# Optimization experiments

Hardware: AMD Instinct MI355X
Metric: run time of the kernel (lower is better)

The kernel has to match this reference:

```python
import jax, jax.numpy as jnp
import numpy as np

N = 100000      # num nodes
E = 1600000     # num edges
DIN, DH, DOUT = 128, 64, 32
BN_EPS = 1e-5


def setup_inputs() -> dict:
    key = jax.random.key(0)
    ks = jax.random.split(key, 6)

    def xavier(k, fi, fo):
        lim = np.sqrt(6.0 / (fi + fo)).astype(np.float32)
        return jax.random.uniform(k, (fi, fo), jnp.float32, -lim, lim)

    return {
        "x": jax.random.normal(ks[0], (N, DIN), jnp.float32),
        "edge_index": jax.random.randint(ks[1], (2, E), 0, N, dtype=jnp.int32),
        "W1": xavier(ks[2], DIN, DH),
        "b1": jnp.zeros((DH,), jnp.float32),
        "gamma1": jnp.ones((DH,), jnp.float32),
        "beta1": jnp.zeros((DH,), jnp.float32),
        "W2": xavier(ks[3], DH, DOUT),
        "b2": jnp.zeros((DOUT,), jnp.float32),
    }


def _gcn_norm(edge_index, n, dtype):
    # add self-loops, then symmetric normalization deg^-1/2[src] * deg^-1/2[dst]
    loop = jnp.arange(n, dtype=edge_index.dtype)
    src = jnp.concatenate([edge_index[0], loop])
    dst = jnp.concatenate([edge_index[1], loop])
    deg = jax.ops.segment_sum(jnp.ones_like(dst, dtype=dtype), dst, num_segments=n)
    dis = 1.0 / jnp.sqrt(deg)  # deg >= 1 due to self-loops
    norm = dis[src] * dis[dst]
    return src, dst, norm


def _gcn_layer(h, W, b, src, dst, norm, n):
    h = h @ W
    msg = h[src] * norm[:, None]                       # [E+N, d] gather
    out = jax.ops.segment_sum(msg, dst, num_segments=n)  # scatter-add
    return out + b


def reference(x, edge_index, W1, b1, gamma1, beta1, W2, b2):
    src, dst, norm = _gcn_norm(edge_index, N, x.dtype)
    # layer 1: GCNConv -> BatchNorm (batch stats) -> ReLU (dropout = eval/identity)
    h = _gcn_layer(x, W1, b1, src, dst, norm, N)
    mean = h.mean(axis=0)
    var = h.var(axis=0)
    h = (h - mean) / jnp.sqrt(var + BN_EPS) * gamma1 + beta1
    h = jax.nn.relu(h)
    # layer 2: GCNConv -> node embeddings [N, DOUT]
    out = _gcn_layer(h, W2, b2, src, dst, norm, N)
    return out
```

## Files before the change

kernel.cpp:

```cpp
#include <hip/hip_runtime.h>

#define DIN 128
#define DH 64
#define DOUT 32
#define BN_EPS 1e-5f

#define BK 128
#define BKSH 7
#define NBK_MAX 784
#define G 512

typedef __attribute__((ext_vector_type(8))) short short8;
typedef __attribute__((ext_vector_type(4))) float floatx4;

__device__ __forceinline__ unsigned short f2bf(float f) {
    union { float f; unsigned u; } v; v.f = f;
    unsigned r = (v.u + 0x7FFFu + ((v.u >> 16) & 1u)) >> 16;
    return (unsigned short)r;
}
__device__ __forceinline__ float bf2f(unsigned short h) {
    union { unsigned u; float f; } v; v.u = ((unsigned)h) << 16;
    return v.f;
}


__global__ __launch_bounds__(256) void wprep_k(const float* __restrict__ W1, const float* __restrict__ W2,
                                               unsigned short* __restrict__ w1t, unsigned short* __restrict__ w2t) {
    int i = blockIdx.x * 256 + threadIdx.x;
    if (i < 8192) {
        int k = i >> 6, nn = i & 63;
        w1t[nn * 128 + k] = f2bf(W1[i]);
    } else if (i < 8192 + 2048) {
        int j = i - 8192;
        int k = j >> 5, nn = j & 31;
        w2t[nn * 64 + k] = f2bf(W2[j]);
    }
}


__global__ __launch_bounds__(256) void hist_k(const int* __restrict__ dst, int* __restrict__ hist_g,
                                              int E, int nbk, int chunk) {
    __shared__ int hist[NBK_MAX];
    int g = blockIdx.x, tid = threadIdx.x;
    for (int b = tid; b < nbk; b += 256) hist[b] = 0;
    __syncthreads();
    int i0 = g * chunk, iend = min(i0 + chunk, E);
    for (int i = i0 + tid; i < iend; i += 256)
        atomicAdd(&hist[dst[i] >> BKSH], 1);
    __syncthreads();
    for (int b = tid; b < nbk; b += 256)
        hist_g[(size_t)g * nbk + b] = hist[b];
}


__global__ __launch_bounds__(256) void scan_k(const int* __restrict__ hist_g, int* __restrict__ rowoff,
                                              int* __restrict__ tot, int nbk) {
    __shared__ int sa[G], sb[G];
    int b = blockIdx.x, tid = threadIdx.x;
    int v0 = hist_g[(size_t)tid * nbk + b];
    int v1 = hist_g[(size_t)(tid + 256) * nbk + b];
    sa[tid] = v0; sa[tid + 256] = v1;
    __syncthreads();
    int* pin = sa; int* pout = sb;
    for (int off = 1; off < G; off <<= 1) {
        int a0 = pin[tid] + ((tid >= off) ? pin[tid - off] : 0);
        int a1 = pin[tid + 256] + ((tid + 256 >= off) ? pin[tid + 256 - off] : 0);
        pout[tid] = a0; pout[tid + 256] = a1;
        __syncthreads();
        int* t = pin; pin = pout; pout = t;
    }
    rowoff[(size_t)b * G + tid] = pin[tid] - v0;
    rowoff[(size_t)b * G + tid + 256] = pin[tid + 256] - v1;
    if (tid == 0) tot[b] = pin[G - 1];
}


__global__ __launch_bounds__(1024) void base_k(const int* __restrict__ tot, int* __restrict__ base,
                                               int nbk, int E) {
    __shared__ int sa[1024], sb[1024];
    int tid = threadIdx.x;
    int v = (tid < nbk) ? tot[tid] : 0;
    sa[tid] = v;
    __syncthreads();
    int* pin = sa; int* pout = sb;
    for (int off = 1; off < 1024; off <<= 1) {
        int a = pin[tid] + ((tid >= off) ? pin[tid - off] : 0);
        pout[tid] = a;
        __syncthreads();
        int* t = pin; pin = pout; pout = t;
    }
    if (tid < nbk) base[tid] = pin[tid] - v;
    if (tid == 0) base[nbk] = E;
}


__global__ __launch_bounds__(256) void scatter_k(const int* __restrict__ src, const int* __restrict__ dst,
                                                 const int* __restrict__ base, const int* __restrict__ rowoff,
                                                 unsigned* __restrict__ recs, int E, int nbk, int chunk) {
    __shared__ int cur[NBK_MAX];
    int g = blockIdx.x, tid = threadIdx.x;
    for (int b = tid; b < nbk; b += 256)
        cur[b] = base[b] + rowoff[(size_t)b * G + g];
    __syncthreads();
    int i0 = g * chunk, iend = min(i0 + chunk, E);
    for (int i = i0 + tid; i < iend; i += 256) {
        int s = src[i], d = dst[i];
        int b = d >> BKSH;
        int slot = atomicAdd(&cur[b], 1);
        recs[slot] = ((unsigned)s << BKSH) | (unsigned)(d & (BK - 1));
    }
}


__global__ __launch_bounds__(256) void csr_k(const unsigned* __restrict__ recs, const int* __restrict__ base,
                                             float* __restrict__ dis, int2* __restrict__ rpde,
                                             int* __restrict__ col, int n) {
    __shared__ int deg[BK], bas[BK], cur[BK], sc[BK];
    int b = blockIdx.x, tid = threadIdx.x;
    if (tid < BK) { deg[tid] = 0; cur[tid] = 0; }
    __syncthreads();
    int lo = base[b], hi = base[b + 1];
    for (int e = lo + tid; e < hi; e += 256)
        atomicAdd(&deg[recs[e] & (BK - 1)], 1);
    __syncthreads();
    if (tid < BK) sc[tid] = deg[tid];
    __syncthreads();
    for (int off = 1; off < BK; off <<= 1) {
        int t = (tid >= off && tid < BK) ? sc[tid - off] : 0;
        __syncthreads();
        if (tid < BK) sc[tid] += t;
        __syncthreads();
    }
    if (tid < BK) {
        bas[tid] = sc[tid] - deg[tid];
        int g = b * BK + tid;
        if (g < n) {
            dis[g] = rsqrtf((float)(deg[tid] + 1));
            rpde[g] = make_int2(lo + bas[tid], deg[tid]);
        }
    }
    __syncthreads();
    for (int e = lo + tid; e < hi; e += 256) {
        unsigned r = recs[e];
        int dl = r & (BK - 1);
        int k = atomicAdd(&cur[dl], 1);
        col[lo + bas[dl] + k] = (int)(r >> BKSH);
    }
}


__global__ __launch_bounds__(256) void gemm1_k(const float* __restrict__ x,
                                               const unsigned short* __restrict__ w1t,
                                               const float* __restrict__ dis,
                                               unsigned short* __restrict__ h1s, int n) {
    __shared__ unsigned short xb[64][136];
    __shared__ unsigned short wt[64][136];
    int tid = threadIdx.x;
    int r0b = blockIdx.x * 64;

    for (int c = tid; c < 1024; c += 256) {
        int nn = c >> 4, kc = (c & 15) * 8;
        *(short8*)&wt[nn][kc] = *(const short8*)&w1t[nn * 128 + kc];
    }
    for (int c = tid; c < 2048; c += 256) {
        int r = c >> 5, k4 = (c & 31) * 4;
        int gr = r0b + r;
        float4 v = make_float4(0.f, 0.f, 0.f, 0.f);
        if (gr < n) v = ((const float4*)x)[(gr << 5) + (k4 >> 2)];
        ushort4 o;
        o.x = f2bf(v.x); o.y = f2bf(v.y); o.z = f2bf(v.z); o.w = f2bf(v.w);
        *(ushort4*)&xb[r][k4] = o;
    }
    __syncthreads();

    int w = tid >> 6, lane = tid & 63;
    int rr = lane & 15, q = lane >> 4;
    floatx4 acc0 = {0.f, 0.f, 0.f, 0.f}, acc1 = acc0, acc2 = acc0, acc3 = acc0;
    #pragma unroll
    for (int kt = 0; kt < 4; kt++) {
        int k0 = kt * 32 + q * 8;
        short8 a  = *(const short8*)&xb[w * 16 + rr][k0];
        short8 b0 = *(const short8*)&wt[rr][k0];
        short8 b1 = *(const short8*)&wt[16 + rr][k0];
        short8 b2 = *(const short8*)&wt[32 + rr][k0];
        short8 b3 = *(const short8*)&wt[48 + rr][k0];
        acc0 = __builtin_amdgcn_mfma_f32_16x16x32_bf16(a, b0, acc0, 0, 0, 0);
        acc1 = __builtin_amdgcn_mfma_f32_16x16x32_bf16(a, b1, acc1, 0, 0, 0);
        acc2 = __builtin_amdgcn_mfma_f32_16x16x32_bf16(a, b2, acc2, 0, 0, 0);
        acc3 = __builtin_amdgcn_mfma_f32_16x16x32_bf16(a, b3, acc3, 0, 0, 0);
    }
    #pragma unroll
    for (int t = 0; t < 4; t++) {
        int gr = r0b + w * 16 + q * 4 + t;
        if (gr < n) {
            float dd = dis[gr];
            unsigned short* o = &h1s[gr * 64];
            o[rr]      = f2bf(acc0[t] * dd);
            o[16 + rr] = f2bf(acc1[t] * dd);
            o[32 + rr] = f2bf(acc2[t] * dd);
            o[48 + rr] = f2bf(acc3[t] * dd);
        }
    }
}


__global__ __launch_bounds__(256) void agg1_k(const unsigned short* __restrict__ h1s,
                                              const int2* __restrict__ rpde,
                                              const int* __restrict__ col,
                                              unsigned short* __restrict__ out, int n) {
    int node = (blockIdx.x * 256 + threadIdx.x) >> 6;
    int f = threadIdx.x & 63;
    if (node >= n) return;
    int2 rd = rpde[node];
    int e  = __builtin_amdgcn_readfirstlane(rd.x);
    int dg = __builtin_amdgcn_readfirstlane(rd.y);
    int ee = e + dg;
    float a0 = 0.f, a1 = 0.f, a2 = 0.f, a3 = 0.f, a4 = 0.f, a5 = 0.f, a6 = 0.f, a7 = 0.f;
    for (; e + 7 < ee; e += 8) {
        int s0 = col[e],     s1 = col[e + 1], s2 = col[e + 2], s3 = col[e + 3];
        int s4 = col[e + 4], s5 = col[e + 5], s6 = col[e + 6], s7 = col[e + 7];
        a0 += bf2f(h1s[s0 * 64 + f]);
        a1 += bf2f(h1s[s1 * 64 + f]);
        a2 += bf2f(h1s[s2 * 64 + f]);
        a3 += bf2f(h1s[s3 * 64 + f]);
        a4 += bf2f(h1s[s4 * 64 + f]);
        a5 += bf2f(h1s[s5 * 64 + f]);
        a6 += bf2f(h1s[s6 * 64 + f]);
        a7 += bf2f(h1s[s7 * 64 + f]);
    }
    for (; e + 3 < ee; e += 4) {
        int s0 = col[e], s1 = col[e + 1], s2 = col[e + 2], s3 = col[e + 3];
        a0 += bf2f(h1s[s0 * 64 + f]);
        a1 += bf2f(h1s[s1 * 64 + f]);
        a2 += bf2f(h1s[s2 * 64 + f]);
        a3 += bf2f(h1s[s3 * 64 + f]);
    }
    for (; e < ee; e++) a0 += bf2f(h1s[col[e] * 64 + f]);
    float dn = rsqrtf((float)(dg + 1));
    float s = ((a0 + a1) + (a2 + a3)) + ((a4 + a5) + (a6 + a7));
    out[node * 64 + f] = f2bf((s + bf2f(h1s[node * 64 + f])) * dn);
}


__global__ __launch_bounds__(256) void bnstats_k(const unsigned short* __restrict__ agg1b,
                                                 float* __restrict__ stats, int n) {
    int f = threadIdx.x & 63, g = threadIdx.x >> 6;
    float sum = 0.f, sq = 0.f;
    for (int r = blockIdx.x * 4 + g; r < n; r += gridDim.x * 4) {
        float v = bf2f(agg1b[r * 64 + f]);
        sum += v; sq += v * v;
    }
    __shared__ float s1[4][64], s2[4][64];
    s1[g][f] = sum; s2[g][f] = sq;
    __syncthreads();
    if (g == 0) {
        sum = s1[0][f] + s1[1][f] + s1[2][f] + s1[3][f];
        sq  = s2[0][f] + s2[1][f] + s2[2][f] + s2[3][f];
        atomicAdd(&stats[f], sum);
        atomicAdd(&stats[64 + f], sq);
    }
}

__global__ __launch_bounds__(64) void bnfin_k(const float* __restrict__ stats, const float* __restrict__ gamma,
                                              const float* __restrict__ beta, float* __restrict__ st, float invn) {
    int f = threadIdx.x;
    if (f < 64) {
        float mean = stats[f] * invn;
        float var = stats[64 + f] * invn - mean * mean;
        float s = gamma[f] * rsqrtf(var + BN_EPS);
        st[f] = s;
        st[64 + f] = beta[f] - mean * s;
    }
}


__global__ __launch_bounds__(256) void gemm2_k(const unsigned short* __restrict__ agg1b,
                                               const unsigned short* __restrict__ w2t,
                                               const float* __restrict__ st, const float* __restrict__ dis,
                                               unsigned short* __restrict__ h2s, int n) {
    __shared__ unsigned short ab[64][72];
    __shared__ unsigned short wt[32][72];
    __shared__ float s_s[64], s_t[64];
    int tid = threadIdx.x;
    int r0b = blockIdx.x * 64;
    if (tid < 64) { s_s[tid] = st[tid]; s_t[tid] = st[64 + tid]; }
    if (tid < 256) {
        int c = tid;
        int nn = c >> 3, kc = (c & 7) * 8;
        *(short8*)&wt[nn][kc] = *(const short8*)&w2t[nn * 64 + kc];
    }
    __syncthreads();
    for (int c = tid; c < 512; c += 256) {
        int r = c >> 3, k0 = (c & 7) * 8;
        int gr = r0b + r;
        unsigned short tmp[8];
        if (gr < n) {
            const unsigned short* ap = &agg1b[gr * 64 + k0];
            #pragma unroll
            for (int j = 0; j < 8; j++)
                tmp[j] = f2bf(fmaxf(bf2f(ap[j]) * s_s[k0 + j] + s_t[k0 + j], 0.f));
        } else {
            #pragma unroll
            for (int j = 0; j < 8; j++) tmp[j] = 0;
        }
        *(short8*)&ab[r][k0] = *(short8*)tmp;
    }
    __syncthreads();

    int w = tid >> 6, lane = tid & 63;
    int rr = lane & 15, q = lane >> 4;
    floatx4 acc0 = {0.f, 0.f, 0.f, 0.f}, acc1 = acc0;
    #pragma unroll
    for (int kt = 0; kt < 2; kt++) {
        int k0 = kt * 32 + q * 8;
        short8 a  = *(const short8*)&ab[w * 16 + rr][k0];
        short8 b0 = *(const short8*)&wt[rr][k0];
        short8 b1 = *(const short8*)&wt[16 + rr][k0];
        acc0 = __builtin_amdgcn_mfma_f32_16x16x32_bf16(a, b0, acc0, 0, 0, 0);
        acc1 = __builtin_amdgcn_mfma_f32_16x16x32_bf16(a, b1, acc1, 0, 0, 0);
    }
    #pragma unroll
    for (int t = 0; t < 4; t++) {
        int gr = r0b + w * 16 + q * 4 + t;
        if (gr < n) {
            float dd = dis[gr];
            h2s[gr * 32 + rr]      = f2bf(acc0[t] * dd);
            h2s[gr * 32 + 16 + rr] = f2bf(acc1[t] * dd);
        }
    }
}


__global__ __launch_bounds__(256) void agg2_k(const unsigned short* __restrict__ h2s,
                                              const int2* __restrict__ rpde,
                                              const int* __restrict__ col, const float* __restrict__ b2,
                                              float* __restrict__ out, int n) {
    int node = (blockIdx.x * 256 + threadIdx.x) >> 6;
    int lane = threadIdx.x & 63;
    if (node >= n) return;
    int f = lane & 31, half = lane >> 5;
    int2 rd = rpde[node];
    int e0 = __builtin_amdgcn_readfirstlane(rd.x);
    int dg = __builtin_amdgcn_readfirstlane(rd.y);
    int e = e0 + half, ee = e0 + dg;
    float a0 = 0.f, a1 = 0.f, a2 = 0.f, a3 = 0.f, a4 = 0.f, a5 = 0.f, a6 = 0.f, a7 = 0.f;
    for (; e + 14 < ee; e += 16) {
        int s0 = col[e],      s1 = col[e + 2],  s2 = col[e + 4],  s3 = col[e + 6];
        int s4 = col[e + 8],  s5 = col[e + 10], s6 = col[e + 12], s7 = col[e + 14];
        a0 += bf2f(h2s[s0 * 32 + f]);
        a1 += bf2f(h2s[s1 * 32 + f]);
        a2 += bf2f(h2s[s2 * 32 + f]);
        a3 += bf2f(h2s[s3 * 32 + f]);
        a4 += bf2f(h2s[s4 * 32 + f]);
        a5 += bf2f(h2s[s5 * 32 + f]);
        a6 += bf2f(h2s[s6 * 32 + f]);
        a7 += bf2f(h2s[s7 * 32 + f]);
    }
    for (; e < ee; e += 2) a0 += bf2f(h2s[col[e] * 32 + f]);
    float acc = ((a0 + a1) + (a2 + a3)) + ((a4 + a5) + (a6 + a7));
    acc += __shfl_down(acc, 32, 64);
    if (half == 0) {
        float dn = rsqrtf((float)(dg + 1));
        out[node * 32 + f] = (acc + bf2f(h2s[node * 32 + f])) * dn + b2[f];
    }
}


extern "C" void kernel_launch(void* const* d_in, const int* in_sizes, int n_in,
                              void* d_out, int out_size, void* d_ws, size_t ws_size,
                              hipStream_t stream) {
    const float* x      = (const float*)d_in[0];
    const int*   ei     = (const int*)d_in[1];
    const float* W1     = (const float*)d_in[2];
    const float* gamma1 = (const float*)d_in[4];
    const float* beta1  = (const float*)d_in[5];
    const float* W2     = (const float*)d_in[6];
    const float* b2     = (const float*)d_in[7];
    float* out = (float*)d_out;

    int N = in_sizes[0] / DIN;
    int E = in_sizes[1] / 2;
    const int* src = ei;
    const int* dst = ei + E;
    int nbk = (N + BK - 1) >> BKSH;
    int chunk = (E + G - 1) / G;

    size_t off = 0;
    auto alloc = [&](size_t elems) -> void* {
        void* p = (char*)d_ws + off * 4;
        off += (elems + 127) & ~size_t(127);
        return p;
    };
    int*            hist_g = (int*)alloc((size_t)G * NBK_MAX);
    int*            rowoff = (int*)alloc((size_t)NBK_MAX * G);
    int*            tot    = (int*)alloc(NBK_MAX);
    int*            base   = (int*)alloc(NBK_MAX + 1);
    unsigned*       recs   = (unsigned*)alloc((size_t)E);
    int*            col    = (int*)alloc((size_t)E);
    float*          dis    = (float*)alloc(N);
    int2*           rpde   = (int2*)alloc((size_t)N * 2);
    float*          stats  = (float*)alloc(128);
    float*          st     = (float*)alloc(128);
    unsigned short* w1t    = (unsigned short*)alloc(4096);
    unsigned short* w2t    = (unsigned short*)alloc(1024);
    unsigned short* h1s    = (unsigned short*)alloc((size_t)N * DH / 2);
    unsigned short* agg1b  = (unsigned short*)alloc((size_t)N * DH / 2);
    unsigned short* h2s    = h1s;

    hipMemsetAsync(stats, 0, 128 * sizeof(float), stream);

    wprep_k<<<40, 256, 0, stream>>>(W1, W2, w1t, w2t);
    hist_k<<<G, 256, 0, stream>>>(dst, hist_g, E, nbk, chunk);
    scan_k<<<nbk, 256, 0, stream>>>(hist_g, rowoff, tot, nbk);
    base_k<<<1, 1024, 0, stream>>>(tot, base, nbk, E);
    scatter_k<<<G, 256, 0, stream>>>(src, dst, base, rowoff, recs, E, nbk, chunk);
    csr_k<<<nbk, 256, 0, stream>>>(recs, base, dis, rpde, col, N);

    gemm1_k<<<(N + 63) / 64, 256, 0, stream>>>(x, w1t, dis, h1s, N);
    agg1_k<<<(N + 3) / 4, 256, 0, stream>>>(h1s, rpde, col, agg1b, N);

    bnstats_k<<<400, 256, 0, stream>>>(agg1b, stats, N);
    bnfin_k<<<1, 64, 0, stream>>>(stats, gamma1, beta1, st, 1.0f / (float)N);

    gemm2_k<<<(N + 63) / 64, 256, 0, stream>>>(agg1b, w2t, st, dis, h2s, N);
    agg2_k<<<(N + 3) / 4, 256, 0, stream>>>(h2s, rpde, col, b2, out, N);
}
```

Baseline: 295.7 us.

## Map two nodes per wave in agg2 and use clamped 8-wide tail gathers

The layer-2 aggregation now assigns each half-wave its own destination node, replacing the old scheme where both halves split one node's edges and then combined them with a shuffle. This halves the number of waves launched. Both aggregation kernels also replace their scalar remainder loops with a single 8-wide gather that clamps indices and masks the extra values, so tail edges are fetched in parallel. The risk is divergence between the two halves of a wave when their nodes have different degrees, plus the redundant loads issued for masked tail slots.

Result: faster. 268.2 us (-9.3%).

```diff
diff --git a/kernel.cpp b/kernel.cpp
--- a/kernel.cpp
+++ b/kernel.cpp
@@ -214,11 +214,12 @@
     int2 rd = rpde[node];
     int e  = __builtin_amdgcn_readfirstlane(rd.x);
     int dg = __builtin_amdgcn_readfirstlane(rd.y);
-    int ee = e + dg;
     float a0 = 0.f, a1 = 0.f, a2 = 0.f, a3 = 0.f, a4 = 0.f, a5 = 0.f, a6 = 0.f, a7 = 0.f;
-    for (; e + 7 < ee; e += 8) {
-        int s0 = col[e],     s1 = col[e + 1], s2 = col[e + 2], s3 = col[e + 3];
-        int s4 = col[e + 4], s5 = col[e + 5], s6 = col[e + 6], s7 = col[e + 7];
+    int full = dg & ~7;
+    int b = 0;
+    for (; b < full; b += 8) {
+        int s0 = col[e + b],     s1 = col[e + b + 1], s2 = col[e + b + 2], s3 = col[e + b + 3];
+        int s4 = col[e + b + 4], s5 = col[e + b + 5], s6 = col[e + b + 6], s7 = col[e + b + 7];
         a0 += bf2f(h1s[s0 * 64 + f]);
         a1 += bf2f(h1s[s1 * 64 + f]);
         a2 += bf2f(h1s[s2 * 64 + f]);
@@ -228,14 +229,25 @@
         a6 += bf2f(h1s[s6 * 64 + f]);
         a7 += bf2f(h1s[s7 * 64 + f]);
     }
-    for (; e + 3 < ee; e += 4) {
-        int s0 = col[e], s1 = col[e + 1], s2 = col[e + 2], s3 = col[e + 3];
-        a0 += bf2f(h1s[s0 * 64 + f]);
-        a1 += bf2f(h1s[s1 * 64 + f]);
-        a2 += bf2f(h1s[s2 * 64 + f]);
-        a3 += bf2f(h1s[s3 * 64 + f]);
-    }
-    for (; e < ee; e++) a0 += bf2f(h1s[col[e] * 64 + f]);
+    if (b < dg) {
+        int last = dg - 1;
+        int s0 = col[e + min(b + 0, last)], s1 = col[e + min(b + 1, last)];
+        int s2 = col[e + min(b + 2, last)], s3 = col[e + min(b + 3, last)];
+        int s4 = col[e + min(b + 4, last)], s5 = col[e + min(b + 5, last)];
+        int s6 = col[e + min(b + 6, last)], s7 = col[e + min(b + 7, last)];
+        float v0 = bf2f(h1s[s0 * 64 + f]), v1 = bf2f(h1s[s1 * 64 + f]);
+        float v2 = bf2f(h1s[s2 * 64 + f]), v3 = bf2f(h1s[s3 * 64 + f]);
+        float v4 = bf2f(h1s[s4 * 64 + f]), v5 = bf2f(h1s[s5 * 64 + f]);
+        float v6 = bf2f(h1s[s6 * 64 + f]), v7 = bf2f(h1s[s7 * 64 + f]);
+        a0 += v0;
+        a1 += (b + 1 < dg) ? v1 : 0.f;
+        a2 += (b + 2 < dg) ? v2 : 0.f;
+        a3 += (b + 3 < dg) ? v3 : 0.f;
+        a4 += (b + 4 < dg) ? v4 : 0.f;
+        a5 += (b + 5 < dg) ? v5 : 0.f;
+        a6 += (b + 6 < dg) ? v6 : 0.f;
+        a7 += (b + 7 < dg) ? v7 : 0.f;
+    }
     float dn = rsqrtf((float)(dg + 1));
     float s = ((a0 + a1) + (a2 + a3)) + ((a4 + a5) + (a6 + a7));
     out[node * 64 + f] = f2bf((s + bf2f(h1s[node * 64 + f])) * dn);
@@ -335,18 +347,19 @@
                                               const int2* __restrict__ rpde,
                                               const int* __restrict__ col, const float* __restrict__ b2,
                                               float* __restrict__ out, int n) {
-    int node = (blockIdx.x * 256 + threadIdx.x) >> 6;
+    int wave = (blockIdx.x * 256 + threadIdx.x) >> 6;
     int lane = threadIdx.x & 63;
+    int f = lane & 31, half = lane >> 5;
+    int node = wave * 2 + half;
     if (node >= n) return;
-    int f = lane & 31, half = lane >> 5;
     int2 rd = rpde[node];
-    int e0 = __builtin_amdgcn_readfirstlane(rd.x);
-    int dg = __builtin_amdgcn_readfirstlane(rd.y);
-    int e = e0 + half, ee = e0 + dg;
+    int e = rd.x, dg = rd.y;
     float a0 = 0.f, a1 = 0.f, a2 = 0.f, a3 = 0.f, a4 = 0.f, a5 = 0.f, a6 = 0.f, a7 = 0.f;
-    for (; e + 14 < ee; e += 16) {
-        int s0 = col[e],      s1 = col[e + 2],  s2 = col[e + 4],  s3 = col[e + 6];
-        int s4 = col[e + 8],  s5 = col[e + 10], s6 = col[e + 12], s7 = col[e + 14];
+    int full = dg & ~7;
+    int b = 0;
+    for (; b < full; b += 8) {
+        int s0 = col[e + b],     s1 = col[e + b + 1], s2 = col[e + b + 2], s3 = col[e + b + 3];
+        int s4 = col[e + b + 4], s5 = col[e + b + 5], s6 = col[e + b + 6], s7 = col[e + b + 7];
         a0 += bf2f(h2s[s0 * 32 + f]);
         a1 += bf2f(h2s[s1 * 32 + f]);
         a2 += bf2f(h2s[s2 * 32 + f]);
@@ -356,13 +369,28 @@
         a6 += bf2f(h2s[s6 * 32 + f]);
         a7 += bf2f(h2s[s7 * 32 + f]);
     }
-    for (; e < ee; e += 2) a0 += bf2f(h2s[col[e] * 32 + f]);
+    if (b < dg) {
+        int last = dg - 1;
+        int s0 = col[e + min(b + 0, last)], s1 = col[e + min(b + 1, last)];
+        int s2 = col[e + min(b + 2, last)], s3 = col[e + min(b + 3, last)];
+        int s4 = col[e + min(b + 4, last)], s5 = col[e + min(b + 5, last)];
+        int s6 = col[e + min(b + 6, last)], s7 = col[e + min(b + 7, last)];
+        float v0 = bf2f(h2s[s0 * 32 + f]), v1 = bf2f(h2s[s1 * 32 + f]);
+        float v2 = bf2f(h2s[s2 * 32 + f]), v3 = bf2f(h2s[s3 * 32 + f]);
+        float v4 = bf2f(h2s[s4 * 32 + f]), v5 = bf2f(h2s[s5 * 32 + f]);
+        float v6 = bf2f(h2s[s6 * 32 + f]), v7 = bf2f(h2s[s7 * 32 + f]);
+        a0 += v0;
+        a1 += (b + 1 < dg) ? v1 : 0.f;
+        a2 += (b + 2 < dg) ? v2 : 0.f;
+        a3 += (b + 3 < dg) ? v3 : 0.f;
+        a4 += (b + 4 < dg) ? v4 : 0.f;
+        a5 += (b + 5 < dg) ? v5 : 0.f;
+        a6 += (b + 6 < dg) ? v6 : 0.f;
+        a7 += (b + 7 < dg) ? v7 : 0.f;
+    }
     float acc = ((a0 + a1) + (a2 + a3)) + ((a4 + a5) + (a6 + a7));
-    acc += __shfl_down(acc, 32, 64);
-    if (half == 0) {
-        float dn = rsqrtf((float)(dg + 1));
-        out[node * 32 + f] = (acc + bf2f(h2s[node * 32 + f])) * dn + b2[f];
-    }
+    float dn = rsqrtf((float)(dg + 1));
+    out[node * 32 + f] = (acc + bf2f(h2s[node * 32 + f])) * dn + b2[f];
 }
 
 
@@ -423,5 +451,5 @@
     bnfin_k<<<1, 64, 0, stream>>>(stats, gamma1, beta1, st, 1.0f / (float)N);
 
     gemm2_k<<<(N + 63) / 64, 256, 0, stream>>>(agg1b, w2t, st, dis, h2s, N);
-    agg2_k<<<(N + 3) / 4, 256, 0, stream>>>(h2s, rpde, col, b2, out, N);
-}
+    agg2_k<<<(N + 7) / 8, 256, 0, stream>>>(h2s, rpde, col, b2, out, N);
+}
```

## Vectorize bf16 gathers to 32-bit pairs in aggregation kernels and fold BN finalize into GEMM2

Applied to the files above, without the earlier changes.

Both aggregation kernels now load two bf16 features per 32-bit gather, so half of each wave handles alternate edges and the two halves are combined with a shuffle. agg2 now packs two nodes per wave. Tails are handled with clamped, predicated loads rather than scalar loops. The separate batch-norm finalize kernel is removed and its per-feature math is recomputed inside each gemm2 block, which drops one launch and adds a small amount of redundant work per block.

Result: faster. 260.8 us (-11.8%).

```diff
diff --git a/kernel.cpp b/kernel.cpp
--- a/kernel.cpp
+++ b/kernel.cpp
@@ -21,6 +21,17 @@
 __device__ __forceinline__ float bf2f(unsigned short h) {
     union { unsigned u; float f; } v; v.u = ((unsigned)h) << 16;
     return v.f;
+}
+__device__ __forceinline__ float lo_f(unsigned u) {
+    union { unsigned u; float f; } v; v.u = u << 16;
+    return v.f;
+}
+__device__ __forceinline__ float hi_f(unsigned u) {
+    union { unsigned u; float f; } v; v.u = u & 0xFFFF0000u;
+    return v.f;
+}
+__device__ __forceinline__ unsigned pack2bf(float lo, float hi) {
+    return (unsigned)f2bf(lo) | ((unsigned)f2bf(hi) << 16);
 }
 
 
@@ -204,41 +215,69 @@
 }
 
 
-__global__ __launch_bounds__(256) void agg1_k(const unsigned short* __restrict__ h1s,
+__global__ __launch_bounds__(256) void agg1_k(const unsigned* __restrict__ h1p,
                                               const int2* __restrict__ rpde,
                                               const int* __restrict__ col,
-                                              unsigned short* __restrict__ out, int n) {
+                                              unsigned* __restrict__ outp, int n) {
     int node = (blockIdx.x * 256 + threadIdx.x) >> 6;
-    int f = threadIdx.x & 63;
+    int lane = threadIdx.x & 63;
     if (node >= n) return;
+    int f2 = lane & 31, eslot = lane >> 5;
     int2 rd = rpde[node];
     int e  = __builtin_amdgcn_readfirstlane(rd.x);
     int dg = __builtin_amdgcn_readfirstlane(rd.y);
-    int ee = e + dg;
-    float a0 = 0.f, a1 = 0.f, a2 = 0.f, a3 = 0.f, a4 = 0.f, a5 = 0.f, a6 = 0.f, a7 = 0.f;
-    for (; e + 7 < ee; e += 8) {
-        int s0 = col[e],     s1 = col[e + 1], s2 = col[e + 2], s3 = col[e + 3];
-        int s4 = col[e + 4], s5 = col[e + 5], s6 = col[e + 6], s7 = col[e + 7];
-        a0 += bf2f(h1s[s0 * 64 + f]);
-        a1 += bf2f(h1s[s1 * 64 + f]);
-        a2 += bf2f(h1s[s2 * 64 + f]);
-        a3 += bf2f(h1s[s3 * 64 + f]);
-        a4 += bf2f(h1s[s4 * 64 + f]);
-        a5 += bf2f(h1s[s5 * 64 + f]);
-        a6 += bf2f(h1s[s6 * 64 + f]);
-        a7 += bf2f(h1s[s7 * 64 + f]);
-    }
-    for (; e + 3 < ee; e += 4) {
-        int s0 = col[e], s1 = col[e + 1], s2 = col[e + 2], s3 = col[e + 3];
-        a0 += bf2f(h1s[s0 * 64 + f]);
-        a1 += bf2f(h1s[s1 * 64 + f]);
-        a2 += bf2f(h1s[s2 * 64 + f]);
-        a3 += bf2f(h1s[s3 * 64 + f]);
-    }
-    for (; e < ee; e++) a0 += bf2f(h1s[col[e] * 64 + f]);
-    float dn = rsqrtf((float)(dg + 1));
-    float s = ((a0 + a1) + (a2 + a3)) + ((a4 + a5) + (a6 + a7));
-    out[node * 64 + f] = f2bf((s + bf2f(h1s[node * 64 + f])) * dn);
+
+    float lo0 = 0.f, lo1 = 0.f, lo2 = 0.f, lo3 = 0.f, lo4 = 0.f, lo5 = 0.f, lo6 = 0.f, lo7 = 0.f;
+    float hi0 = 0.f, hi1 = 0.f, hi2 = 0.f, hi3 = 0.f, hi4 = 0.f, hi5 = 0.f, hi6 = 0.f, hi7 = 0.f;
+    int b = 0;
+    for (; b + 16 <= dg; b += 16) {
+        int s0 = col[e + b + 0 + eslot],  s1 = col[e + b + 2 + eslot];
+        int s2 = col[e + b + 4 + eslot],  s3 = col[e + b + 6 + eslot];
+        int s4 = col[e + b + 8 + eslot],  s5 = col[e + b + 10 + eslot];
+        int s6 = col[e + b + 12 + eslot], s7 = col[e + b + 14 + eslot];
+        unsigned u0 = h1p[s0 * 32 + f2], u1 = h1p[s1 * 32 + f2];
+        unsigned u2 = h1p[s2 * 32 + f2], u3 = h1p[s3 * 32 + f2];
+        unsigned u4 = h1p[s4 * 32 + f2], u5 = h1p[s5 * 32 + f2];
+        unsigned u6 = h1p[s6 * 32 + f2], u7 = h1p[s7 * 32 + f2];
+        lo0 += lo_f(u0); hi0 += hi_f(u0);
+        lo1 += lo_f(u1); hi1 += hi_f(u1);
+        lo2 += lo_f(u2); hi2 += hi_f(u2);
+        lo3 += lo_f(u3); hi3 += hi_f(u3);
+        lo4 += lo_f(u4); hi4 += hi_f(u4);
+        lo5 += lo_f(u5); hi5 += hi_f(u5);
+        lo6 += lo_f(u6); hi6 += hi_f(u6);
+        lo7 += lo_f(u7); hi7 += hi_f(u7);
+    }
+    if (b < dg) {
+        int last = dg - 1;
+        int i0 = b + 0 + eslot,  i1 = b + 2 + eslot,  i2 = b + 4 + eslot,  i3 = b + 6 + eslot;
+        int i4 = b + 8 + eslot,  i5 = b + 10 + eslot, i6 = b + 12 + eslot, i7 = b + 14 + eslot;
+        int s0 = col[e + min(i0, last)], s1 = col[e + min(i1, last)];
+        int s2 = col[e + min(i2, last)], s3 = col[e + min(i3, last)];
+        int s4 = col[e + min(i4, last)], s5 = col[e + min(i5, last)];
+        int s6 = col[e + min(i6, last)], s7 = col[e + min(i7, last)];
+        unsigned u0 = h1p[s0 * 32 + f2], u1 = h1p[s1 * 32 + f2];
+        unsigned u2 = h1p[s2 * 32 + f2], u3 = h1p[s3 * 32 + f2];
+        unsigned u4 = h1p[s4 * 32 + f2], u5 = h1p[s5 * 32 + f2];
+        unsigned u6 = h1p[s6 * 32 + f2], u7 = h1p[s7 * 32 + f2];
+        lo0 += (i0 < dg) ? lo_f(u0) : 0.f; hi0 += (i0 < dg) ? hi_f(u0) : 0.f;
+        lo1 += (i1 < dg) ? lo_f(u1) : 0.f; hi1 += (i1 < dg) ? hi_f(u1) : 0.f;
+        lo2 += (i2 < dg) ? lo_f(u2) : 0.f; hi2 += (i2 < dg) ? hi_f(u2) : 0.f;
+        lo3 += (i3 < dg) ? lo_f(u3) : 0.f; hi3 += (i3 < dg) ? hi_f(u3) : 0.f;
+        lo4 += (i4 < dg) ? lo_f(u4) : 0.f; hi4 += (i4 < dg) ? hi_f(u4) : 0.f;
+        lo5 += (i5 < dg) ? lo_f(u5) : 0.f; hi5 += (i5 < dg) ? hi_f(u5) : 0.f;
+        lo6 += (i6 < dg) ? lo_f(u6) : 0.f; hi6 += (i6 < dg) ? hi_f(u6) : 0.f;
+        lo7 += (i7 < dg) ? lo_f(u7) : 0.f; hi7 += (i7 < dg) ? hi_f(u7) : 0.f;
+    }
+    float lo = ((lo0 + lo1) + (lo2 + lo3)) + ((lo4 + lo5) + (lo6 + lo7));
+    float hi = ((hi0 + hi1) + (hi2 + hi3)) + ((hi4 + hi5) + (hi6 + hi7));
+    lo += __shfl_xor(lo, 32, 64);
+    hi += __shfl_xor(hi, 32, 64);
+    if (eslot == 0) {
+        unsigned us = h1p[node * 32 + f2];
+        float dn = rsqrtf((float)(dg + 1));
+        outp[node * 32 + f2] = pack2bf((lo + lo_f(us)) * dn, (hi + hi_f(us)) * dn);
+    }
 }
 
 
@@ -261,29 +300,25 @@
     }
 }
 
-__global__ __launch_bounds__(64) void bnfin_k(const float* __restrict__ stats, const float* __restrict__ gamma,
-                                              const float* __restrict__ beta, float* __restrict__ st, float invn) {
-    int f = threadIdx.x;
-    if (f < 64) {
-        float mean = stats[f] * invn;
-        float var = stats[64 + f] * invn - mean * mean;
-        float s = gamma[f] * rsqrtf(var + BN_EPS);
-        st[f] = s;
-        st[64 + f] = beta[f] - mean * s;
-    }
-}
-
 
 __global__ __launch_bounds__(256) void gemm2_k(const unsigned short* __restrict__ agg1b,
                                                const unsigned short* __restrict__ w2t,
-                                               const float* __restrict__ st, const float* __restrict__ dis,
-                                               unsigned short* __restrict__ h2s, int n) {
+                                               const float* __restrict__ stats,
+                                               const float* __restrict__ gamma, const float* __restrict__ beta,
+                                               const float* __restrict__ dis,
+                                               unsigned short* __restrict__ h2s, float invn, int n) {
     __shared__ unsigned short ab[64][72];
     __shared__ unsigned short wt[32][72];
     __shared__ float s_s[64], s_t[64];
     int tid = threadIdx.x;
     int r0b = blockIdx.x * 64;
-    if (tid < 64) { s_s[tid] = st[tid]; s_t[tid] = st[64 + tid]; }
+    if (tid < 64) {
+        float mean = stats[tid] * invn;
+        float var = stats[64 + tid] * invn - mean * mean;
+        float s = gamma[tid] * rsqrtf(var + BN_EPS);
+        s_s[tid] = s;
+        s_t[tid] = beta[tid] - mean * s;
+    }
     if (tid < 256) {
         int c = tid;
         int nn = c >> 3, kc = (c & 7) * 8;
@@ -331,37 +366,73 @@
 }
 
 
-__global__ __launch_bounds__(256) void agg2_k(const unsigned short* __restrict__ h2s,
+__global__ __launch_bounds__(256) void agg2_k(const unsigned* __restrict__ h2p,
                                               const int2* __restrict__ rpde,
                                               const int* __restrict__ col, const float* __restrict__ b2,
                                               float* __restrict__ out, int n) {
-    int node = (blockIdx.x * 256 + threadIdx.x) >> 6;
+    int wave = (blockIdx.x * 256 + threadIdx.x) >> 6;
     int lane = threadIdx.x & 63;
+    int half = lane >> 5, hl = lane & 31;
+    int node = wave * 2 + half;
     if (node >= n) return;
-    int f = lane & 31, half = lane >> 5;
+    int f2 = hl & 15, eslot = hl >> 4;
     int2 rd = rpde[node];
-    int e0 = __builtin_amdgcn_readfirstlane(rd.x);
-    int dg = __builtin_amdgcn_readfirstlane(rd.y);
-    int e = e0 + half, ee = e0 + dg;
-    float a0 = 0.f, a1 = 0.f, a2 = 0.f, a3 = 0.f, a4 = 0.f, a5 = 0.f, a6 = 0.f, a7 = 0.f;
-    for (; e + 14 < ee; e += 16) {
-        int s0 = col[e],      s1 = col[e + 2],  s2 = col[e + 4],  s3 = col[e + 6];
-        int s4 = col[e + 8],  s5 = col[e + 10], s6 = col[e + 12], s7 = col[e + 14];
-        a0 += bf2f(h2s[s0 * 32 + f]);
-        a1 += bf2f(h2s[s1 * 32 + f]);
-        a2 += bf2f(h2s[s2 * 32 + f]);
-        a3 += bf2f(h2s[s3 * 32 + f]);
-        a4 += bf2f(h2s[s4 * 32 + f]);
-        a5 += bf2f(h2s[s5 * 32 + f]);
-        a6 += bf2f(h2s[s6 * 32 + f]);
-        a7 += bf2f(h2s[s7 * 32 + f]);
-    }
-    for (; e < ee; e += 2) a0 += bf2f(h2s[col[e] * 32 + f]);
-    float acc = ((a0 + a1) + (a2 + a3)) + ((a4 + a5) + (a6 + a7));
-    acc += __shfl_down(acc, 32, 64);
-    if (half == 0) {
+    int e = rd.x, dg = rd.y;
+
+    float lo0 = 0.f, lo1 = 0.f, lo2 = 0.f, lo3 = 0.f, lo4 = 0.f, lo5 = 0.f, lo6 = 0.f, lo7 = 0.f;
+    float hi0 = 0.f, hi1 = 0.f, hi2 = 0.f, hi3 = 0.f, hi4 = 0.f, hi5 = 0.f, hi6 = 0.f, hi7 = 0.f;
+    int b = 0;
+    for (; b + 16 <= dg; b += 16) {
+        int s0 = col[e + b + 0 + eslot],  s1 = col[e + b + 2 + eslot];
+        int s2 = col[e + b + 4 + eslot],  s3 = col[e + b + 6 + eslot];
+        int s4 = col[e + b + 8 + eslot],  s5 = col[e + b + 10 + eslot];
+        int s6 = col[e + b + 12 + eslot], s7 = col[e + b + 14 + eslot];
+        unsigned u0 = h2p[s0 * 16 + f2], u1 = h2p[s1 * 16 + f2];
+        unsigned u2 = h2p[s2 * 16 + f2], u3 = h2p[s3 * 16 + f2];
+        unsigned u4 = h2p[s4 * 16 + f2], u5 = h2p[s5 * 16 + f2];
+        unsigned u6 = h2p[s6 * 16 + f2], u7 = h2p[s7 * 16 + f2];
+        lo0 += lo_f(u0); hi0 += hi_f(u0);
+        lo1 += lo_f(u1); hi1 += hi_f(u1);
+        lo2 += lo_f(u2); hi2 += hi_f(u2);
+        lo3 += lo_f(u3); hi3 += hi_f(u3);
+        lo4 += lo_f(u4); hi4 += hi_f(u4);
+        lo5 += lo_f(u5); hi5 += hi_f(u5);
+        lo6 += lo_f(u6); hi6 += hi_f(u6);
+        lo7 += lo_f(u7); hi7 += hi_f(u7);
+    }
+    if (b < dg) {
+        int last = dg - 1;
+        int i0 = b + 0 + eslot,  i1 = b + 2 + eslot,  i2 = b + 4 + eslot,  i3 = b + 6 + eslot;
+        int i4 = b + 8 + eslot,  i5 = b + 10 + eslot, i6 = b + 12 + eslot, i7 = b + 14 + eslot;
+        int s0 = col[e + min(i0, last)], s1 = col[e + min(i1, last)];
+        int s2 = col[e + min(i2, last)], s3 = col[e + min(i3, last)];
+        int s4 = col[e + min(i4, last)], s5 = col[e + min(i5, last)];
+        int s6 = col[e + min(i6, last)], s7 = col[e + min(i7, last)];
+        unsigned u0 = h2p[s0 * 16 + f2], u1 = h2p[s1 * 16 + f2];
+        unsigned u2 = h2p[s2 * 16 + f2], u3 = h2p[s3 * 16 + f2];
+        unsigned u4 = h2p[s4 * 16 + f2], u5 = h2p[s5 * 16 + f2];
+        unsigned u6 = h2p[s6 * 16 + f2], u7 = h2p[s7 * 16 + f2];
+        lo0 += (i0 < dg) ? lo_f(u0) : 0.f; hi0 += (i0 < dg) ? hi_f(u0) : 0.f;
+        lo1 += (i1 < dg) ? lo_f(u1) : 0.f; hi1 += (i1 < dg) ? hi_f(u1) : 0.f;
+        lo2 += (i2 < dg) ? lo_f(u2) : 0.f; hi2 += (i2 < dg) ? hi_f(u2) : 0.f;
+        lo3 += (i3 < dg) ? lo_f(u3) : 0.f; hi3 += (i3 < dg) ? hi_f(u3) : 0.f;
+        lo4 += (i4 < dg) ? lo_f(u4) : 0.f; hi4 += (i4 < dg) ? hi_f(u4) : 0.f;
+        lo5 += (i5 < dg) ? lo_f(u5) : 0.f; hi5 += (i5 < dg) ? hi_f(u5) : 0.f;
+        lo6 += (i6 < dg) ? lo_f(u6) : 0.f; hi6 += (i6 < dg) ? hi_f(u6) : 0.f;
+        lo7 += (i7 < dg) ? lo_f(u7) : 0.f; hi7 += (i7 < dg) ? hi_f(u7) : 0.f;
+    }
+    float lo = ((lo0 + lo1) + (lo2 + lo3)) + ((lo4 + lo5) + (lo6 + lo7));
+    float hi = ((hi0 + hi1) + (hi2 + hi3)) + ((hi4 + hi5) + (hi6 + hi7));
+    lo += __shfl_xor(lo, 16, 64);
+    hi += __shfl_xor(hi, 16, 64);
+    if (eslot == 0) {
+        unsigned us = h2p[node * 16 + f2];
         float dn = rsqrtf((float)(dg + 1));
-        out[node * 32 + f] = (acc + bf2f(h2s[node * 32 + f])) * dn + b2[f];
+        float2 bb = ((const float2*)b2)[f2];
+        float2 o;
+        o.x = (lo + lo_f(us)) * dn + bb.x;
+        o.y = (hi + hi_f(us)) * dn + bb.y;
+        ((float2*)out)[node * 16 + f2] = o;
     }
 }
 
@@ -400,7 +471,6 @@
     float*          dis    = (float*)alloc(N);
     int2*           rpde   = (int2*)alloc((size_t)N * 2);
     float*          stats  = (float*)alloc(128);
-    float*          st     = (float*)alloc(128);
     unsigned short* w1t    = (unsigned short*)alloc(4096);
     unsigned short* w2t    = (unsigned short*)alloc(1024);
     unsigned short* h1s    = (unsigned short*)alloc((size_t)N * DH / 2);
@@ -417,11 +487,11 @@
     csr_k<<<nbk, 256, 0, stream>>>(recs, base, dis, rpde, col, N);
 
     gemm1_k<<<(N + 63) / 64, 256, 0, stream>>>(x, w1t, dis, h1s, N);
-    agg1_k<<<(N + 3) / 4, 256, 0, stream>>>(h1s, rpde, col, agg1b, N);
+    agg1_k<<<(N + 3) / 4, 256, 0, stream>>>((const unsigned*)h1s, rpde, col, (unsigned*)agg1b, N);
 
     bnstats_k<<<400, 256, 0, stream>>>(agg1b, stats, N);
-    bnfin_k<<<1, 64, 0, stream>>>(stats, gamma1, beta1, st, 1.0f / (float)N);
-
-    gemm2_k<<<(N + 63) / 64, 256, 0, stream>>>(agg1b, w2t, st, dis, h2s, N);
-    agg2_k<<<(N + 3) / 4, 256, 0, stream>>>(h2s, rpde, col, b2, out, N);
-}
+
+    gemm2_k<<<(N + 63) / 64, 256, 0, stream>>>(agg1b, w2t, stats, gamma1, beta1, dis, h2s,
+                                               1.0f / (float)N, N);
+    agg2_k<<<(N + 7) / 8, 256, 0, stream>>>((const unsigned*)h2s, rpde, col, b2, out, N);
+}
```
